# Optimization experiments

Hardware: AMD Instinct MI355X
Metric: run time of the kernel (lower is better)

Reference implementation:

```python
import jax, jax.numpy as jnp
import numpy as np

NEG_SLOPE = 0.01  # torch F.leaky_relu default


def _graph_conv(x, W, b, src, dst, n_dst):
    """DGL GraphConv, norm='both': out = D_dst^{-1/2} A^T (D_src^{-1/2} x W) + b.
    Degrees clamped to min 1 (DGL behavior). src/dst are edge endpoint indices.
    """
    n_src = x.shape[0]
    ones = jnp.ones(src.shape[0], dtype=x.dtype)
    out_deg = jnp.zeros(n_src, dtype=x.dtype).at[src].add(ones)
    in_deg = jnp.zeros(n_dst, dtype=x.dtype).at[dst].add(ones)
    inv_s = jax.lax.rsqrt(jnp.maximum(out_deg, 1.0))
    inv_d = jax.lax.rsqrt(jnp.maximum(in_deg, 1.0))
    # weight first (in_feats >= out_feats path in DGL; math identical either way)
    feat = (x * inv_s[:, None]) @ W                      # [n_src, out]
    agg = jax.ops.segment_sum(feat[src], dst, num_segments=n_dst)  # SpMM
    return agg * inv_d[:, None] + b


def setup_inputs() -> dict:
    key = jax.random.key(0)
    ks = jax.random.split(key, 16)
    Nc, Ng, F, H, O = 50000, 30000, 128, 128, 128
    Ecc, Ecg, Egc = 500000, 400000, 400000
    inp = {
        "x_chem": jax.random.normal(ks[0], (Nc, F), jnp.float32),
        "x_gene": jax.random.normal(ks[1], (Ng, F), jnp.float32),
        "src_cc": jax.random.randint(ks[2], (Ecc,), 0, Nc, jnp.int32),
        "dst_cc": jax.random.randint(ks[3], (Ecc,), 0, Nc, jnp.int32),
        "src_cg": jax.random.randint(ks[4], (Ecg,), 0, Nc, jnp.int32),
        "dst_cg": jax.random.randint(ks[5], (Ecg,), 0, Ng, jnp.int32),
        "src_gc": jax.random.randint(ks[6], (Egc,), 0, Ng, jnp.int32),
        "dst_gc": jax.random.randint(ks[7], (Egc,), 0, Nc, jnp.int32),
    }
    scale1 = 1.0 / np.sqrt(F)
    scale2 = 1.0 / np.sqrt(H)
    inp["W1_cc"] = jax.random.normal(ks[8], (F, H), jnp.float32) * scale1
    inp["W1_cg"] = jax.random.normal(ks[9], (F, H), jnp.float32) * scale1
    inp["W1_gc"] = jax.random.normal(ks[10], (F, H), jnp.float32) * scale1
    inp["W2_cc"] = jax.random.normal(ks[11], (H, O), jnp.float32) * scale2
    inp["W2_cg"] = jax.random.normal(ks[12], (H, O), jnp.float32) * scale2
    inp["W2_gc"] = jax.random.normal(ks[13], (H, O), jnp.float32) * scale2
    for name, d in [("b1_cc", H), ("b1_cg", H), ("b1_gc", H), ("b2_cc", O), ("b2_cg", O), ("b2_gc", O)]:
        inp[name] = jnp.zeros((d,), jnp.float32)
    return inp


def reference(x_chem, x_gene, src_cc, dst_cc, src_cg, dst_cg, src_gc, dst_gc,
              W1_cc, b1_cc, W1_cg, b1_cg, W1_gc, b1_gc,
              W2_cc, b2_cc, W2_cg, b2_cg, W2_gc, b2_gc):
    Nc, Ng = x_chem.shape[0], x_gene.shape[0]
    # --- layer 1: HeteroGraphConv with sum aggregation across relations ---
    h1_chem = (_graph_conv(x_chem, W1_cc, b1_cc, src_cc, dst_cc, Nc)
               + _graph_conv(x_gene, W1_gc, b1_gc, src_gc, dst_gc, Nc))
    h1_gene = _graph_conv(x_chem, W1_cg, b1_cg, src_cg, dst_cg, Ng)
    h1_chem = jax.nn.leaky_relu(h1_chem, NEG_SLOPE)
    h1_gene = jax.nn.leaky_relu(h1_gene, NEG_SLOPE)
    # --- layer 2 ---
    h2_chem = (_graph_conv(h1_chem, W2_cc, b2_cc, src_cc, dst_cc, Nc)
               + _graph_conv(h1_gene, W2_gc, b2_gc, src_gc, dst_gc, Nc))
    return h2_chem
```

## Files before the change

kernel.cpp:

```cpp
#include <hip/hip_runtime.h>
#include <math.h>

#define NEG_SLOPE 0.01f
#define ELLW 40

typedef float f4 __attribute__((ext_vector_type(4)));
typedef __bf16 bf16x8 __attribute__((ext_vector_type(8)));
typedef __bf16 bf16x4 __attribute__((ext_vector_type(4)));

__global__ __launch_bounds__(256) void prep_w_zero(
    const float* __restrict__ W0, const float* __restrict__ W1,
    const float* __restrict__ W2, const float* __restrict__ W3,
    const float* __restrict__ W4, __bf16* __restrict__ H, __bf16* __restrict__ L,
    int* __restrict__ zp, int zN)
{
    const int b = blockIdx.x;
    if (b < 320) {
        const int y = b >> 6;
        const float* W = y == 0 ? W0 : y == 1 ? W1 : y == 2 ? W2 : y == 3 ? W3 : W4;
        int idx = (b & 63) * 256 + threadIdx.x;
        int k = idx >> 7, n = idx & 127;
        float w = W[idx];
        __bf16 h = (__bf16)w;
        __bf16 l = (__bf16)(w - (float)h);
        H[(size_t)y * 16384 + n * 128 + k] = h;
        L[(size_t)y * 16384 + n * 128 + k] = l;
    } else {
        int i = (b - 320) * 256 + threadIdx.x;
        if (i < zN) zp[i] = 0;
    }
}

template <int RELU>
__device__ __forceinline__ void gemm_core(const float* __restrict__ A,
    const __bf16* __restrict__ Bh, const __bf16* __restrict__ Bl,
    float* __restrict__ C, int M, int row0, int tid,
    __bf16 (*Ah)[136], __bf16 (*Al)[136])
{
#pragma unroll
    for (int it = 0; it < 8; ++it) {
        int idx4 = it * 256 + tid;
        int r = idx4 >> 5;
        int c = (idx4 & 31) << 2;
        int rg = row0 + r;
        f4 v = {0.f, 0.f, 0.f, 0.f};
        if (rg < M) v = *(const f4*)(A + (size_t)rg * 128 + c);
        if (RELU) {
#pragma unroll
            for (int j = 0; j < 4; ++j) v[j] = v[j] >= 0.f ? v[j] : v[j] * NEG_SLOPE;
        }
        bf16x4 hv, lv;
#pragma unroll
        for (int j = 0; j < 4; ++j) {
            __bf16 h = (__bf16)v[j];
            hv[j] = h;
            lv[j] = (__bf16)(v[j] - (float)h);
        }
        *(bf16x4*)&Ah[r][c] = hv;
        *(bf16x4*)&Al[r][c] = lv;
    }
    __syncthreads();

    const int lane = tid & 63;
    const int wid = tid >> 6;
    const int lm = lane & 15;
    const int lq = lane >> 4;
    const int mbase = (wid & 1) * 32;
    const int nbase = (wid >> 1) * 64;

    f4 acc[2][4] = {};
#pragma unroll
    for (int kc = 0; kc < 4; ++kc) {
        const int koff = kc * 32 + lq * 8;
        bf16x8 ah[2], al[2], bh[4], bl[4];
#pragma unroll
        for (int mi = 0; mi < 2; ++mi) {
            ah[mi] = *(const bf16x8*)&Ah[mbase + mi * 16 + lm][koff];
            al[mi] = *(const bf16x8*)&Al[mbase + mi * 16 + lm][koff];
        }
#pragma unroll
        for (int ni = 0; ni < 4; ++ni) {
            size_t boff = (size_t)(nbase + ni * 16 + lm) * 128 + koff;
            bh[ni] = *(const bf16x8*)(Bh + boff);
            bl[ni] = *(const bf16x8*)(Bl + boff);
        }
#pragma unroll
        for (int mi = 0; mi < 2; ++mi)
#pragma unroll
            for (int ni = 0; ni < 4; ++ni) {
                acc[mi][ni] = __builtin_amdgcn_mfma_f32_16x16x32_bf16(ah[mi], bh[ni], acc[mi][ni], 0, 0, 0);
                acc[mi][ni] = __builtin_amdgcn_mfma_f32_16x16x32_bf16(al[mi], bh[ni], acc[mi][ni], 0, 0, 0);
                acc[mi][ni] = __builtin_amdgcn_mfma_f32_16x16x32_bf16(ah[mi], bl[ni], acc[mi][ni], 0, 0, 0);
            }
    }

#pragma unroll
    for (int mi = 0; mi < 2; ++mi) {
        int rbase = row0 + mbase + mi * 16 + lq * 4;
#pragma unroll
        for (int r = 0; r < 4; ++r) {
            int row = rbase + r;
            if (row < M) {
#pragma unroll
                for (int ni = 0; ni < 4; ++ni)
                    C[(size_t)row * 128 + nbase + ni * 16 + lm] = acc[mi][ni][r];
            }
        }
    }
}

__global__ __launch_bounds__(256) void fused_build_gemm(
    const int* __restrict__ s0, const int* __restrict__ d0, int* sd0, int* c0, int* e0, int E0, int B0,
    const int* __restrict__ s1, const int* __restrict__ d1, int* sd1, int* c1, int* e1, int E1, int B1,
    const int* __restrict__ s2, const int* __restrict__ d2, int* sd2, int* c2, int* e2, int E2,
    const float* __restrict__ xc, const float* __restrict__ xg,
    const __bf16* __restrict__ wt_h, const __bf16* __restrict__ wt_l,
    float* __restrict__ t_cg, float* __restrict__ t_cc, float* __restrict__ t_gc,
    int Nc, int Ng, int gBc, int G, int EB)
{
    __shared__ __bf16 Ah[64][136];
    __shared__ __bf16 Al[64][136];
    const int idx = blockIdx.x;
    const int r7 = idx % 7, q = idx / 7;
    if (r7 < 2) {
        int g = q * 2 + r7;
        if (g >= G) return;
        if (g < gBc)
            gemm_core<0>(xc, wt_h, wt_l, t_cg, Nc, g * 64, threadIdx.x, Ah, Al);
        else if (g < 2 * gBc)
            gemm_core<0>(xc, wt_h + 16384, wt_l + 16384, t_cc, Nc, (g - gBc) * 64, threadIdx.x, Ah, Al);
        else
            gemm_core<0>(xg, wt_h + 2 * 16384, wt_l + 2 * 16384, t_gc, Ng, (g - 2 * gBc) * 64, threadIdx.x, Ah, Al);
    } else {
        int eb = q * 5 + (r7 - 2);
        if (eb >= EB) return;
        const int* src; const int* dst; int* sdeg; int* cnt; int* ell; int E; int base;
        if (eb < B0)            { src = s0; dst = d0; sdeg = sd0; cnt = c0; ell = e0; E = E0; base = eb; }
        else if (eb < B0 + B1)  { src = s1; dst = d1; sdeg = sd1; cnt = c1; ell = e1; E = E1; base = eb - B0; }
        else                    { src = s2; dst = d2; sdeg = sd2; cnt = c2; ell = e2; E = E2; base = eb - B0 - B1; }
        int i = base * 256 + threadIdx.x;
        if (i < E) {
            int s = src[i];
            int d = dst[i];
            atomicAdd(&sdeg[s], 1);
            int p = atomicAdd(&cnt[d], 1);
            if (p < ELLW) ell[d * ELLW + p] = s;
        }
    }
}

__global__ __launch_bounds__(256) void gemm2_both(
    const float* __restrict__ h1c, const float* __restrict__ h1g,
    const __bf16* __restrict__ wt_h, const __bf16* __restrict__ wt_l,
    float* __restrict__ t_cc, float* __restrict__ t_gc, int Nc, int Ng, int gBc)
{
    __shared__ __bf16 Ah[64][136];
    __shared__ __bf16 Al[64][136];
    if ((int)blockIdx.x < gBc)
        gemm_core<1>(h1c, wt_h + 3 * 16384, wt_l + 3 * 16384, t_cc, Nc, blockIdx.x * 64, threadIdx.x, Ah, Al);
    else
        gemm_core<1>(h1g, wt_h + 4 * 16384, wt_l + 4 * 16384, t_gc, Ng, (blockIdx.x - gBc) * 64, threadIdx.x, Ah, Al);
}

__device__ __forceinline__ void rel_accum4(const float* __restrict__ feat,
    const int* __restrict__ cp, int n, const int* __restrict__ sdeg,
    int half, int c4, f4& acc)
{
    int i = half;
    for (; i + 2 < n; i += 4) {
        int q0 = cp[i], q1 = cp[i + 2];
        float w0 = rsqrtf(fmaxf((float)sdeg[q0], 1.0f));
        float w1 = rsqrtf(fmaxf((float)sdeg[q1], 1.0f));
        f4 v0 = *(const f4*)(feat + (size_t)q0 * 128 + c4);
        f4 v1 = *(const f4*)(feat + (size_t)q1 * 128 + c4);
        acc += v0 * w0;
        acc += v1 * w1;
    }
    if (i < n) {
        int q0 = cp[i];
        float w0 = rsqrtf(fmaxf((float)sdeg[q0], 1.0f));
        f4 v0 = *(const f4*)(feat + (size_t)q0 * 128 + c4);
        acc += v0 * w0;
    }
}

__device__ __forceinline__ f4 xhalf_sum(f4 r)
{
    f4 o;
    o[0] = __shfl_xor(r[0], 32);
    o[1] = __shfl_xor(r[1], 32);
    o[2] = __shfl_xor(r[2], 32);
    o[3] = __shfl_xor(r[3], 32);
    return r + o;
}

__global__ __launch_bounds__(256) void gather_l1(
    const float* __restrict__ t_cg, const int* __restrict__ ell_cg,
    const int* __restrict__ cnt_cg, const int* __restrict__ degs_cg,
    const float* __restrict__ f_cc, const int* __restrict__ ell_cc,
    const int* __restrict__ cnt_cc, const int* __restrict__ degs_cc,
    const float* __restrict__ t_gc, const int* __restrict__ ell_gc,
    const int* __restrict__ cnt_gc, const int* __restrict__ degs_gc,
    const float* __restrict__ b1_cg, const float* __restrict__ b1_cc, const float* __restrict__ b1_gc,
    float* __restrict__ h1_gene, float* __restrict__ h1_chem, int Ng, int Nc, int Bg)
{
    const int lane = threadIdx.x & 63;
    const int half = lane >> 5;
    const int c4 = (lane & 31) << 2;
    if ((int)blockIdx.x < Bg) {
        int row = blockIdx.x * 4 + (threadIdx.x >> 6);
        if (row >= Ng) return;
        int n = cnt_cg[row];
        float wd = rsqrtf(fmaxf((float)n, 1.0f));
        if (n > ELLW) n = ELLW;
        f4 acc = {0.f, 0.f, 0.f, 0.f};
        rel_accum4(t_cg, ell_cg + row * ELLW, n, degs_cg, half, c4, acc);
        f4 r = acc * wd;
        r = xhalf_sum(r);
        if (half == 0) {
            r += *(const f4*)(b1_cg + c4);
            *(f4*)(h1_gene + (size_t)row * 128 + c4) = r;
        }
    } else {
        int row = (blockIdx.x - Bg) * 4 + (threadIdx.x >> 6);
        if (row >= Nc) return;
        int na = cnt_cc[row];
        float wa = rsqrtf(fmaxf((float)na, 1.0f));
        if (na > ELLW) na = ELLW;
        f4 accA = {0.f, 0.f, 0.f, 0.f};
        rel_accum4(f_cc, ell_cc + row * ELLW, na, degs_cc, half, c4, accA);
        int nb = cnt_gc[row];
        float wb = rsqrtf(fmaxf((float)nb, 1.0f));
        if (nb > ELLW) nb = ELLW;
        f4 accB = {0.f, 0.f, 0.f, 0.f};
        rel_accum4(t_gc, ell_gc + row * ELLW, nb, degs_gc, half, c4, accB);
        f4 r = accA * wa + accB * wb;
        r = xhalf_sum(r);
        if (half == 0) {
            r += *(const f4*)(b1_cc + c4);
            r += *(const f4*)(b1_gc + c4);
            *(f4*)(h1_chem + (size_t)row * 128 + c4) = r;
        }
    }
}

__global__ __launch_bounds__(256) void gather_l2(
    const float* __restrict__ fA, const int* __restrict__ ellA,
    const int* __restrict__ cntA, const int* __restrict__ degsA,
    const float* __restrict__ fB, const int* __restrict__ ellB,
    const int* __restrict__ cntB, const int* __restrict__ degsB,
    const float* __restrict__ bA, const float* __restrict__ bB,
    float* __restrict__ out, int Nd)
{
    const int lane = threadIdx.x & 63;
    const int half = lane >> 5;
    const int c4 = (lane & 31) << 2;
    int row = blockIdx.x * 4 + (threadIdx.x >> 6);
    if (row >= Nd) return;
    int na = cntA[row];
    float wa = rsqrtf(fmaxf((float)na, 1.0f));
    if (na > ELLW) na = ELLW;
    f4 accA = {0.f, 0.f, 0.f, 0.f};
    rel_accum4(fA, ellA + row * ELLW, na, degsA, half, c4, accA);
    int nb = cntB[row];
    float wb = rsqrtf(fmaxf((float)nb, 1.0f));
    if (nb > ELLW) nb = ELLW;
    f4 accB = {0.f, 0.f, 0.f, 0.f};
    rel_accum4(fB, ellB + row * ELLW, nb, degsB, half, c4, accB);
    f4 r = accA * wa + accB * wb;
    r = xhalf_sum(r);
    if (half == 0) {
        r += *(const f4*)(bA + c4);
        r += *(const f4*)(bB + c4);
        *(f4*)(out + (size_t)row * 128 + c4) = r;
    }
}

extern "C" void kernel_launch(void* const* d_in, const int* in_sizes, int n_in,
                              void* d_out, int out_size, void* d_ws, size_t ws_size,
                              hipStream_t stream)
{
    const float* x_chem = (const float*)d_in[0];
    const float* x_gene = (const float*)d_in[1];
    const int* src_cc = (const int*)d_in[2];
    const int* dst_cc = (const int*)d_in[3];
    const int* src_cg = (const int*)d_in[4];
    const int* dst_cg = (const int*)d_in[5];
    const int* src_gc = (const int*)d_in[6];
    const int* dst_gc = (const int*)d_in[7];
    const float* W1_cc = (const float*)d_in[8];
    const float* W1_cg = (const float*)d_in[9];
    const float* W1_gc = (const float*)d_in[10];
    const float* W2_cc = (const float*)d_in[11];
    const float* W2_gc = (const float*)d_in[13];
    const float* b1_cc = (const float*)d_in[14];
    const float* b1_cg = (const float*)d_in[15];
    const float* b1_gc = (const float*)d_in[16];
    const float* b2_cc = (const float*)d_in[17];
    const float* b2_gc = (const float*)d_in[19];
    (void)n_in; (void)out_size; (void)ws_size;

    const int Nc = in_sizes[0] / 128;
    const int Ng = in_sizes[1] / 128;
    const int Ecc = in_sizes[2];
    const int Ecg = in_sizes[4];
    const int Egc = in_sizes[6];

    int* ip = (int*)d_ws;
    int* cnt_cc  = ip; ip += Nc;
    int* cnt_cg  = ip; ip += Ng;
    int* cnt_gc  = ip; ip += Nc;
    int* degs_cc = ip; ip += Nc;
    int* degs_cg = ip; ip += Nc;
    int* degs_gc = ip; ip += Ng;
    const int degTotal = 4 * Nc + 2 * Ng;
    int* ell_cc = ip; ip += (size_t)Nc * ELLW;
    int* ell_cg = ip; ip += (size_t)Ng * ELLW;
    int* ell_gc = ip; ip += (size_t)Nc * ELLW;
    size_t intCount = (size_t)(ip - (int*)d_ws);
    intCount = (intCount + 3) & ~(size_t)3;
    float* fp = (float*)d_ws + intCount;
    float* h1_chem = fp; fp += (size_t)Nc * 128;
    float* h1_gene = fp; fp += (size_t)Ng * 128;
    float* tmp_cg  = fp; fp += (size_t)Nc * 128;
    float* tmp_gc  = fp; fp += (size_t)Ng * 128;
    __bf16* wt_h = (__bf16*)fp;
    __bf16* wt_l = wt_h + 5 * 16384;
    float* outF = (float*)d_out;

    dim3 blk(256);
    const int B0 = (Ecc + 255) / 256, B1 = (Ecg + 255) / 256, B2 = (Egc + 255) / 256;
    const int EB = B0 + B1 + B2;
    const int gBc = (Nc + 63) / 64, gBg = (Ng + 63) / 64;
    const int G = 2 * gBc + gBg;
    int Q = (G + 1) / 2;
    if ((EB + 4) / 5 > Q) Q = (EB + 4) / 5;
    const int T = 7 * Q;

    const int zB = (degTotal + 255) / 256;
    prep_w_zero<<<320 + zB, blk, 0, stream>>>(W1_cg, W1_cc, W1_gc, W2_cc, W2_gc,
        wt_h, wt_l, (int*)d_ws, degTotal);

    fused_build_gemm<<<T, blk, 0, stream>>>(
        src_cc, dst_cc, degs_cc, cnt_cc, ell_cc, Ecc, B0,
        src_cg, dst_cg, degs_cg, cnt_cg, ell_cg, Ecg, B1,
        src_gc, dst_gc, degs_gc, cnt_gc, ell_gc, Egc,
        x_chem, x_gene, wt_h, wt_l, tmp_cg, outF, tmp_gc,
        Nc, Ng, gBc, G, EB);

    const int Bg = (Ng + 3) / 4, Bc = (Nc + 3) / 4;
    gather_l1<<<Bg + Bc, blk, 0, stream>>>(
        tmp_cg, ell_cg, cnt_cg, degs_cg,
        outF,  ell_cc, cnt_cc, degs_cc,
        tmp_gc, ell_gc, cnt_gc, degs_gc,
        b1_cg, b1_cc, b1_gc, h1_gene, h1_chem, Ng, Nc, Bg);

    gemm2_both<<<gBc + gBg, blk, 0, stream>>>(h1_chem, h1_gene, wt_h, wt_l,
        tmp_cg, tmp_gc, Nc, Ng, gBc);

    gather_l2<<<Bc, blk, 0, stream>>>(
        tmp_cg, ell_cc, cnt_cc, degs_cc,
        tmp_gc, ell_gc, cnt_gc, degs_gc,
        b2_cc, b2_gc, outF, Nc);
}
```

Before: 435.1 us.

## Reschedule stages to overlap edge building, gathers and layer-2 GEMMs across kernels

The fused build+GEMM and gather/GEMM stages are split differently. Stage A runs the layer-1 GEMMs alongside only the cg edge build. Stage B builds the cc/gc edges while the gene gather runs. Stage C runs the chem layer-1 gather alongside a 32-row-tile gene layer-2 GEMM, followed by a separate chem layer-2 GEMM. The goal is to overlap dependent work on different relations rather than serialize whole phases, at the cost of one more launch and an extra temporary buffer.

Result: slower. 470.9 us (+8.2%).

```diff
diff --git a/kernel.cpp b/kernel.cpp
--- a/kernel.cpp
+++ b/kernel.cpp
@@ -31,14 +31,14 @@
     }
 }
 
-template <int RELU>
+template <int RELU, int MI>
 __device__ __forceinline__ void gemm_core(const float* __restrict__ A,
     const __bf16* __restrict__ Bh, const __bf16* __restrict__ Bl,
     float* __restrict__ C, int M, int row0, int tid,
     __bf16 (*Ah)[136], __bf16 (*Al)[136])
 {
 #pragma unroll
-    for (int it = 0; it < 8; ++it) {
+    for (int it = 0; it < MI * 4; ++it) {
         int idx4 = it * 256 + tid;
         int r = idx4 >> 5;
         int c = (idx4 & 31) << 2;
@@ -65,16 +65,16 @@
     const int wid = tid >> 6;
     const int lm = lane & 15;
     const int lq = lane >> 4;
-    const int mbase = (wid & 1) * 32;
+    const int mbase = (wid & 1) * (MI * 16);
     const int nbase = (wid >> 1) * 64;
 
-    f4 acc[2][4] = {};
+    f4 acc[MI][4] = {};
 #pragma unroll
     for (int kc = 0; kc < 4; ++kc) {
         const int koff = kc * 32 + lq * 8;
-        bf16x8 ah[2], al[2], bh[4], bl[4];
-#pragma unroll
-        for (int mi = 0; mi < 2; ++mi) {
+        bf16x8 ah[MI], al[MI], bh[4], bl[4];
+#pragma unroll
+        for (int mi = 0; mi < MI; ++mi) {
             ah[mi] = *(const bf16x8*)&Ah[mbase + mi * 16 + lm][koff];
             al[mi] = *(const bf16x8*)&Al[mbase + mi * 16 + lm][koff];
         }
@@ -85,7 +85,7 @@
             bl[ni] = *(const bf16x8*)(Bl + boff);
         }
 #pragma unroll
-        for (int mi = 0; mi < 2; ++mi)
+        for (int mi = 0; mi < MI; ++mi)
 #pragma unroll
             for (int ni = 0; ni < 4; ++ni) {
                 acc[mi][ni] = __builtin_amdgcn_mfma_f32_16x16x32_bf16(ah[mi], bh[ni], acc[mi][ni], 0, 0, 0);
@@ -95,7 +95,7 @@
     }
 
 #pragma unroll
-    for (int mi = 0; mi < 2; ++mi) {
+    for (int mi = 0; mi < MI; ++mi) {
         int rbase = row0 + mbase + mi * 16 + lq * 4;
 #pragma unroll
         for (int r = 0; r < 4; ++r) {
@@ -109,57 +109,18 @@
     }
 }
 
-__global__ __launch_bounds__(256) void fused_build_gemm(
-    const int* __restrict__ s0, const int* __restrict__ d0, int* sd0, int* c0, int* e0, int E0, int B0,
-    const int* __restrict__ s1, const int* __restrict__ d1, int* sd1, int* c1, int* e1, int E1, int B1,
-    const int* __restrict__ s2, const int* __restrict__ d2, int* sd2, int* c2, int* e2, int E2,
-    const float* __restrict__ xc, const float* __restrict__ xg,
-    const __bf16* __restrict__ wt_h, const __bf16* __restrict__ wt_l,
-    float* __restrict__ t_cg, float* __restrict__ t_cc, float* __restrict__ t_gc,
-    int Nc, int Ng, int gBc, int G, int EB)
-{
-    __shared__ __bf16 Ah[64][136];
-    __shared__ __bf16 Al[64][136];
-    const int idx = blockIdx.x;
-    const int r7 = idx % 7, q = idx / 7;
-    if (r7 < 2) {
-        int g = q * 2 + r7;
-        if (g >= G) return;
-        if (g < gBc)
-            gemm_core<0>(xc, wt_h, wt_l, t_cg, Nc, g * 64, threadIdx.x, Ah, Al);
-        else if (g < 2 * gBc)
-            gemm_core<0>(xc, wt_h + 16384, wt_l + 16384, t_cc, Nc, (g - gBc) * 64, threadIdx.x, Ah, Al);
-        else
-            gemm_core<0>(xg, wt_h + 2 * 16384, wt_l + 2 * 16384, t_gc, Ng, (g - 2 * gBc) * 64, threadIdx.x, Ah, Al);
-    } else {
-        int eb = q * 5 + (r7 - 2);
-        if (eb >= EB) return;
-        const int* src; const int* dst; int* sdeg; int* cnt; int* ell; int E; int base;
-        if (eb < B0)            { src = s0; dst = d0; sdeg = sd0; cnt = c0; ell = e0; E = E0; base = eb; }
-        else if (eb < B0 + B1)  { src = s1; dst = d1; sdeg = sd1; cnt = c1; ell = e1; E = E1; base = eb - B0; }
-        else                    { src = s2; dst = d2; sdeg = sd2; cnt = c2; ell = e2; E = E2; base = eb - B0 - B1; }
-        int i = base * 256 + threadIdx.x;
-        if (i < E) {
-            int s = src[i];
-            int d = dst[i];
-            atomicAdd(&sdeg[s], 1);
-            int p = atomicAdd(&cnt[d], 1);
-            if (p < ELLW) ell[d * ELLW + p] = s;
-        }
-    }
-}
-
-__global__ __launch_bounds__(256) void gemm2_both(
-    const float* __restrict__ h1c, const float* __restrict__ h1g,
-    const __bf16* __restrict__ wt_h, const __bf16* __restrict__ wt_l,
-    float* __restrict__ t_cc, float* __restrict__ t_gc, int Nc, int Ng, int gBc)
-{
-    __shared__ __bf16 Ah[64][136];
-    __shared__ __bf16 Al[64][136];
-    if ((int)blockIdx.x < gBc)
-        gemm_core<1>(h1c, wt_h + 3 * 16384, wt_l + 3 * 16384, t_cc, Nc, blockIdx.x * 64, threadIdx.x, Ah, Al);
-    else
-        gemm_core<1>(h1g, wt_h + 4 * 16384, wt_l + 4 * 16384, t_gc, Ng, (blockIdx.x - gBc) * 64, threadIdx.x, Ah, Al);
+__device__ __forceinline__ void build_edges(const int* __restrict__ src,
+    const int* __restrict__ dst, int* __restrict__ sdeg, int* __restrict__ cnt,
+    int* __restrict__ ell, int E, int base, int tid)
+{
+    int i = base * 256 + tid;
+    if (i < E) {
+        int s = src[i];
+        int d = dst[i];
+        atomicAdd(&sdeg[s], 1);
+        int p = atomicAdd(&cnt[d], 1);
+        if (p < ELLW) ell[d * ELLW + p] = s;
+    }
 }
 
 __device__ __forceinline__ void rel_accum4(const float* __restrict__ feat,
@@ -194,69 +155,17 @@
     return r + o;
 }
 
-__global__ __launch_bounds__(256) void gather_l1(
-    const float* __restrict__ t_cg, const int* __restrict__ ell_cg,
-    const int* __restrict__ cnt_cg, const int* __restrict__ degs_cg,
-    const float* __restrict__ f_cc, const int* __restrict__ ell_cc,
-    const int* __restrict__ cnt_cc, const int* __restrict__ degs_cc,
-    const float* __restrict__ t_gc, const int* __restrict__ ell_gc,
-    const int* __restrict__ cnt_gc, const int* __restrict__ degs_gc,
-    const float* __restrict__ b1_cg, const float* __restrict__ b1_cc, const float* __restrict__ b1_gc,
-    float* __restrict__ h1_gene, float* __restrict__ h1_chem, int Ng, int Nc, int Bg)
-{
-    const int lane = threadIdx.x & 63;
-    const int half = lane >> 5;
-    const int c4 = (lane & 31) << 2;
-    if ((int)blockIdx.x < Bg) {
-        int row = blockIdx.x * 4 + (threadIdx.x >> 6);
-        if (row >= Ng) return;
-        int n = cnt_cg[row];
-        float wd = rsqrtf(fmaxf((float)n, 1.0f));
-        if (n > ELLW) n = ELLW;
-        f4 acc = {0.f, 0.f, 0.f, 0.f};
-        rel_accum4(t_cg, ell_cg + row * ELLW, n, degs_cg, half, c4, acc);
-        f4 r = acc * wd;
-        r = xhalf_sum(r);
-        if (half == 0) {
-            r += *(const f4*)(b1_cg + c4);
-            *(f4*)(h1_gene + (size_t)row * 128 + c4) = r;
-        }
-    } else {
-        int row = (blockIdx.x - Bg) * 4 + (threadIdx.x >> 6);
-        if (row >= Nc) return;
-        int na = cnt_cc[row];
-        float wa = rsqrtf(fmaxf((float)na, 1.0f));
-        if (na > ELLW) na = ELLW;
-        f4 accA = {0.f, 0.f, 0.f, 0.f};
-        rel_accum4(f_cc, ell_cc + row * ELLW, na, degs_cc, half, c4, accA);
-        int nb = cnt_gc[row];
-        float wb = rsqrtf(fmaxf((float)nb, 1.0f));
-        if (nb > ELLW) nb = ELLW;
-        f4 accB = {0.f, 0.f, 0.f, 0.f};
-        rel_accum4(t_gc, ell_gc + row * ELLW, nb, degs_gc, half, c4, accB);
-        f4 r = accA * wa + accB * wb;
-        r = xhalf_sum(r);
-        if (half == 0) {
-            r += *(const f4*)(b1_cc + c4);
-            r += *(const f4*)(b1_gc + c4);
-            *(f4*)(h1_chem + (size_t)row * 128 + c4) = r;
-        }
-    }
-}
-
-__global__ __launch_bounds__(256) void gather_l2(
+__device__ __forceinline__ void dual_gather_row(
     const float* __restrict__ fA, const int* __restrict__ ellA,
     const int* __restrict__ cntA, const int* __restrict__ degsA,
     const float* __restrict__ fB, const int* __restrict__ ellB,
     const int* __restrict__ cntB, const int* __restrict__ degsB,
     const float* __restrict__ bA, const float* __restrict__ bB,
-    float* __restrict__ out, int Nd)
-{
-    const int lane = threadIdx.x & 63;
+    float* __restrict__ out, int row, int tid)
+{
+    const int lane = tid & 63;
     const int half = lane >> 5;
     const int c4 = (lane & 31) << 2;
-    int row = blockIdx.x * 4 + (threadIdx.x >> 6);
-    if (row >= Nd) return;
     int na = cntA[row];
     float wa = rsqrtf(fmaxf((float)na, 1.0f));
     if (na > ELLW) na = ELLW;
@@ -274,6 +183,114 @@
         r += *(const f4*)(bB + c4);
         *(f4*)(out + (size_t)row * 128 + c4) = r;
     }
+}
+
+__global__ __launch_bounds__(256) void fused_A(
+    const int* __restrict__ s1, const int* __restrict__ d1,
+    int* sd1, int* c1, int* e1, int E1, int B1,
+    const float* __restrict__ xc, const float* __restrict__ xg,
+    const __bf16* __restrict__ wt_h, const __bf16* __restrict__ wt_l,
+    float* __restrict__ t_cg, float* __restrict__ t_cc, float* __restrict__ t_gc,
+    int Nc, int Ng, int gBc, int G)
+{
+    __shared__ __bf16 Ah[64][136];
+    __shared__ __bf16 Al[64][136];
+    const int r2 = blockIdx.x & 1, q = blockIdx.x >> 1;
+    if (r2 == 0) {
+        if (q >= G) return;
+        if (q < gBc)
+            gemm_core<0, 2>(xc, wt_h, wt_l, t_cg, Nc, q * 64, threadIdx.x, Ah, Al);
+        else if (q < 2 * gBc)
+            gemm_core<0, 2>(xc, wt_h + 16384, wt_l + 16384, t_cc, Nc, (q - gBc) * 64, threadIdx.x, Ah, Al);
+        else
+            gemm_core<0, 2>(xg, wt_h + 2 * 16384, wt_l + 2 * 16384, t_gc, Ng, (q - 2 * gBc) * 64, threadIdx.x, Ah, Al);
+    } else {
+        if (q >= B1) return;
+        build_edges(s1, d1, sd1, c1, e1, E1, q, threadIdx.x);
+    }
+}
+
+__global__ __launch_bounds__(256) void fused_B(
+    const int* __restrict__ s0, const int* __restrict__ d0, int* sd0, int* c0, int* e0, int E0, int B0,
+    const int* __restrict__ s2, const int* __restrict__ d2, int* sd2, int* c2, int* e2, int E2, int B2,
+    const float* __restrict__ t_cg, const int* __restrict__ ell_cg,
+    const int* __restrict__ cnt_cg, const int* __restrict__ degs_cg,
+    const float* __restrict__ b1_cg, float* __restrict__ h1_gene, int Ng, int Bg)
+{
+    const int r3 = blockIdx.x % 3, q = blockIdx.x / 3;
+    if (r3 == 0) {
+        if (q < B0) build_edges(s0, d0, sd0, c0, e0, E0, q, threadIdx.x);
+        else if (q < B0 + B2) build_edges(s2, d2, sd2, c2, e2, E2, q - B0, threadIdx.x);
+    } else {
+        int g = q * 2 + (r3 - 1);
+        if (g >= Bg) return;
+        int row = g * 4 + ((int)threadIdx.x >> 6);
+        if (row >= Ng) return;
+        const int lane = threadIdx.x & 63;
+        const int half = lane >> 5;
+        const int c4 = (lane & 31) << 2;
+        int n = cnt_cg[row];
+        float wd = rsqrtf(fmaxf((float)n, 1.0f));
+        if (n > ELLW) n = ELLW;
+        f4 acc = {0.f, 0.f, 0.f, 0.f};
+        rel_accum4(t_cg, ell_cg + row * ELLW, n, degs_cg, half, c4, acc);
+        f4 r = acc * wd;
+        r = xhalf_sum(r);
+        if (half == 0) {
+            r += *(const f4*)(b1_cg + c4);
+            *(f4*)(h1_gene + (size_t)row * 128 + c4) = r;
+        }
+    }
+}
+
+__global__ __launch_bounds__(256) void fused_C(
+    const float* __restrict__ f_cc, const int* __restrict__ ell_cc,
+    const int* __restrict__ cnt_cc, const int* __restrict__ degs_cc,
+    const float* __restrict__ t_gc, const int* __restrict__ ell_gc,
+    const int* __restrict__ cnt_gc, const int* __restrict__ degs_gc,
+    const float* __restrict__ b1_cc, const float* __restrict__ b1_gc,
+    float* __restrict__ h1_chem, int Nc, int Bc,
+    const float* __restrict__ h1_gene, const __bf16* __restrict__ wt_h,
+    const __bf16* __restrict__ wt_l, float* __restrict__ t2_gc, int Ng, int gBg32)
+{
+    __shared__ __bf16 Ah[32][136];
+    __shared__ __bf16 Al[32][136];
+    const int r14 = blockIdx.x % 14, q = blockIdx.x / 14;
+    if (r14 == 0) {
+        if (q >= gBg32) return;
+        gemm_core<1, 1>(h1_gene, wt_h + 4 * 16384, wt_l + 4 * 16384, t2_gc, Ng, q * 32, threadIdx.x, Ah, Al);
+    } else {
+        int g = q * 13 + (r14 - 1);
+        if (g >= Bc) return;
+        int row = g * 4 + ((int)threadIdx.x >> 6);
+        if (row >= Nc) return;
+        dual_gather_row(f_cc, ell_cc, cnt_cc, degs_cc,
+                        t_gc, ell_gc, cnt_gc, degs_gc,
+                        b1_cc, b1_gc, h1_chem, row, threadIdx.x);
+    }
+}
+
+__global__ __launch_bounds__(256) void gemm2_cc(const float* __restrict__ h1c,
+    const __bf16* __restrict__ wt_h, const __bf16* __restrict__ wt_l,
+    float* __restrict__ t2_cc, int Nc)
+{
+    __shared__ __bf16 Ah[64][136];
+    __shared__ __bf16 Al[64][136];
+    gemm_core<1, 2>(h1c, wt_h + 3 * 16384, wt_l + 3 * 16384, t2_cc, Nc, blockIdx.x * 64, threadIdx.x, Ah, Al);
+}
+
+__global__ __launch_bounds__(256) void gather_l2(
+    const float* __restrict__ fA, const int* __restrict__ ellA,
+    const int* __restrict__ cntA, const int* __restrict__ degsA,
+    const float* __restrict__ fB, const int* __restrict__ ellB,
+    const int* __restrict__ cntB, const int* __restrict__ degsB,
+    const float* __restrict__ bA, const float* __restrict__ bB,
+    float* __restrict__ out, int Nd)
+{
+    int row = blockIdx.x * 4 + ((int)threadIdx.x >> 6);
+    if (row >= Nd) return;
+    dual_gather_row(fA, ellA, cntA, degsA, fB, ellB, cntB, degsB,
+                    bA, bB, out, row, threadIdx.x);
 }
 
 extern "C" void kernel_launch(void* const* d_in, const int* in_sizes, int n_in,
@@ -322,44 +339,54 @@
     float* fp = (float*)d_ws + intCount;
     float* h1_chem = fp; fp += (size_t)Nc * 128;
     float* h1_gene = fp; fp += (size_t)Ng * 128;
-    float* tmp_cg  = fp; fp += (size_t)Nc * 128;
-    float* tmp_gc  = fp; fp += (size_t)Ng * 128;
+    float* t_cg    = fp; fp += (size_t)Nc * 128;
+    float* t_gc    = fp; fp += (size_t)Ng * 128;
+    float* t2_gc   = fp; fp += (size_t)Ng * 128;
     __bf16* wt_h = (__bf16*)fp;
     __bf16* wt_l = wt_h + 5 * 16384;
     float* outF = (float*)d_out;
+    float* t2_cc = t_cg;
 
     dim3 blk(256);
     const int B0 = (Ecc + 255) / 256, B1 = (Ecg + 255) / 256, B2 = (Egc + 255) / 256;
-    const int EB = B0 + B1 + B2;
     const int gBc = (Nc + 63) / 64, gBg = (Ng + 63) / 64;
     const int G = 2 * gBc + gBg;
-    int Q = (G + 1) / 2;
-    if ((EB + 4) / 5 > Q) Q = (EB + 4) / 5;
-    const int T = 7 * Q;
+    const int gBg32 = (Ng + 31) / 32;
+    const int Bg = (Ng + 3) / 4, Bc = (Nc + 3) / 4;
 
     const int zB = (degTotal + 255) / 256;
     prep_w_zero<<<320 + zB, blk, 0, stream>>>(W1_cg, W1_cc, W1_gc, W2_cc, W2_gc,
         wt_h, wt_l, (int*)d_ws, degTotal);
 
-    fused_build_gemm<<<T, blk, 0, stream>>>(
-        src_cc, dst_cc, degs_cc, cnt_cc, ell_cc, Ecc, B0,
-        src_cg, dst_cg, degs_cg, cnt_cg, ell_cg, Ecg, B1,
-        src_gc, dst_gc, degs_gc, cnt_gc, ell_gc, Egc,
-        x_chem, x_gene, wt_h, wt_l, tmp_cg, outF, tmp_gc,
-        Nc, Ng, gBc, G, EB);
-
-    const int Bg = (Ng + 3) / 4, Bc = (Nc + 3) / 4;
-    gather_l1<<<Bg + Bc, blk, 0, stream>>>(
-        tmp_cg, ell_cg, cnt_cg, degs_cg,
-        outF,  ell_cc, cnt_cc, degs_cc,
-        tmp_gc, ell_gc, cnt_gc, degs_gc,
-        b1_cg, b1_cc, b1_gc, h1_gene, h1_chem, Ng, Nc, Bg);
-
-    gemm2_both<<<gBc + gBg, blk, 0, stream>>>(h1_chem, h1_gene, wt_h, wt_l,
-        tmp_cg, tmp_gc, Nc, Ng, gBc);
+    {
+        int Q = G > B1 ? G : B1;
+        fused_A<<<2 * Q, blk, 0, stream>>>(
+            src_cg, dst_cg, degs_cg, cnt_cg, ell_cg, Ecg, B1,
+            x_chem, x_gene, wt_h, wt_l, t_cg, outF, t_gc, Nc, Ng, gBc, G);
+    }
+
+    {
+        int EBb = B0 + B2;
+        int Q = EBb > (Bg + 1) / 2 ? EBb : (Bg + 1) / 2;
+        fused_B<<<3 * Q, blk, 0, stream>>>(
+            src_cc, dst_cc, degs_cc, cnt_cc, ell_cc, Ecc, B0,
+            src_gc, dst_gc, degs_gc, cnt_gc, ell_gc, Egc, B2,
+            t_cg, ell_cg, cnt_cg, degs_cg, b1_cg, h1_gene, Ng, Bg);
+    }
+
+    {
+        int Q = gBg32 > (Bc + 12) / 13 ? gBg32 : (Bc + 12) / 13;
+        fused_C<<<14 * Q, blk, 0, stream>>>(
+            outF, ell_cc, cnt_cc, degs_cc,
+            t_gc, ell_gc, cnt_gc, degs_gc,
+            b1_cc, b1_gc, h1_chem, Nc, Bc,
+            h1_gene, wt_h, wt_l, t2_gc, Ng, gBg32);
+    }
+
+    gemm2_cc<<<gBc, blk, 0, stream>>>(h1_chem, wt_h, wt_l, t2_cc, Nc);
 
     gather_l2<<<Bc, blk, 0, stream>>>(
-        tmp_cg, ell_cc, cnt_cc, degs_cc,
-        tmp_gc, ell_gc, cnt_gc, degs_gc,
+        t2_cc, ell_cc, cnt_cc, degs_cc,
+        t2_gc, ell_gc, cnt_gc, degs_gc,
         b2_cc, b2_gc, outF, Nc);
 }
```
